# Performance work log

Hardware: AMD Instinct MI355X
Metric: run time of the kernel (lower is better)

Reference implementation:

```python
import jax, jax.numpy as jnp
import numpy as np

NUM_HEADS = 8
EPS = 1e-6


def setup_inputs() -> dict:
    key0 = jax.random.key(0)
    ks = jax.random.split(key0, 12)
    B, E, Hs, Ws, L = 8, 512, 32, 32, 1024
    s = 0.02
    return {
        "query": jax.random.normal(ks[0], (B, E, Hs, Ws), dtype=jnp.float32),
        "key": jax.random.normal(ks[1], (B, L, E), dtype=jnp.float32),
        "value": jax.random.normal(ks[2], (B, L, E), dtype=jnp.float32),
        # 1x1 conv for Q (kernel_size=1) stored as (E_out, E_in)
        "Wq": jax.random.normal(ks[3], (E, E), dtype=jnp.float32) * s,
        "bq": jnp.zeros((E,), dtype=jnp.float32),
        "Wk": jax.random.normal(ks[4], (E, E), dtype=jnp.float32) * s,
        "bk": jnp.zeros((E,), dtype=jnp.float32),
        "Wv": jax.random.normal(ks[5], (E, E), dtype=jnp.float32) * s,
        "bv": jnp.zeros((E,), dtype=jnp.float32),
        # out_conv: 1x1 conv + RMSNorm gain
        "Wo": jax.random.normal(ks[6], (E, E), dtype=jnp.float32) * s,
        "bo": jnp.zeros((E,), dtype=jnp.float32),
        "g": jnp.ones((E,), dtype=jnp.float32),
    }


def reference(query, key, value, Wq, bq, Wk, bk, Wv, bv, Wo, bo, g):
    B, E, Hs, Ws = query.shape
    H = NUM_HEADS
    Dh = E // H
    N = Hs * Ws
    # Q: 1x1 conv == per-pixel linear over channels
    Q = jnp.einsum('oi,bihw->bohw', Wq, query) + bq[None, :, None, None]
    # K, V: linear on last dim
    K = key @ Wk.T + bk      # (B, L, E)
    V = value @ Wv.T + bv    # (B, L, E)
    # faithful to torch .view: row-major reshape then transpose(2,3)
    Qh = Q.reshape(B, H, Dh, N).transpose(0, 1, 3, 2)        # (B, H, N, Dh)
    Kh = K.reshape(B, H, Dh, -1).transpose(0, 1, 3, 2)       # (B, H, L, Dh)
    Vh = V.reshape(B, H, Dh, -1).transpose(0, 1, 3, 2)       # (B, H, L, Dh)
    scores = jnp.einsum('bhnd,bhmd->bhnm', Qh, Kh) / jnp.sqrt(jnp.float32(Dh))
    attn = jax.nn.softmax(scores, axis=-1)
    out = jnp.einsum('bhnm,bhmd->bhnd', attn, Vh)            # (B, H, N, Dh)
    out = out.transpose(0, 1, 3, 2).reshape(B, E, Hs, Ws)
    # out_conv: 1x1 conv then channel-wise RMSNorm
    out = jnp.einsum('oi,bihw->bohw', Wo, out) + bo[None, :, None, None]
    rms = jnp.sqrt(jnp.mean(out * out, axis=1, keepdims=True) + EPS)
    return out / rms * g[None, :, None, None]
```

## Files before the change

### kernel.cpp

```cpp
#include <hip/hip_runtime.h>
#include <hip/hip_bf16.h>

namespace {

constexpr int kB  = 8;
constexpr int kE  = 512;
constexpr int kH  = 8;
constexpr int kDh = 64;
constexpr int kN  = 1024;
constexpr int kL  = 1024;

typedef __attribute__((ext_vector_type(8))) short short8;
typedef __attribute__((ext_vector_type(4))) float f32x4;
typedef __attribute__((ext_vector_type(4))) unsigned short ushort4v;

__device__ __forceinline__ unsigned short f2bf(float f) {
  unsigned u = __builtin_bit_cast(unsigned, f);
  u = (u + 0x7fffu + ((u >> 16) & 1u)) >> 16;
  return (unsigned short)u;
}

__device__ __forceinline__ f32x4 mfma16(short8 a, short8 b, f32x4 c) {
  return __builtin_amdgcn_mfma_f32_16x16x32_bf16(a, b, c, 0, 0, 0);
}

__device__ __forceinline__ void gl_lds16(const unsigned short* g, unsigned short* l) {
  __builtin_amdgcn_global_load_lds(
      (const __attribute__((address_space(1))) unsigned int*)g,
      (__attribute__((address_space(3))) unsigned int*)l, 16, 0, 0);
}

__global__ __launch_bounds__(256)
void convert_w(const float* __restrict__ w0, const float* __restrict__ w1,
               const float* __restrict__ w2, const float* __restrict__ w3,
               unsigned short* __restrict__ dst)
{
  const float* s = (blockIdx.y == 0) ? w0 : (blockIdx.y == 1) ? w1
                  : (blockIdx.y == 2) ? w2 : w3;
  unsigned short* d = dst + (size_t)blockIdx.y * 262144;
  const size_t i = ((size_t)blockIdx.x * 256 + threadIdx.x) * 4;
  const float4 v = *(const float4*)(s + i);
  ushort4v o = { f2bf(v.x), f2bf(v.y), f2bf(v.z), f2bf(v.w) };
  *(ushort4v*)(d + i) = o;
}

__global__ __launch_bounds__(256)
void convert_kv(const float* __restrict__ k, const float* __restrict__ v,
                unsigned short* __restrict__ dst)
{
  const float* s = blockIdx.y ? v : k;
  unsigned short* d = dst + (size_t)blockIdx.y * 4194304;
  const int flat = blockIdx.x * 256 + threadIdx.x;
  #pragma unroll
  for (int it = 0; it < 4; ++it) {
    const size_t i = ((size_t)flat + (size_t)it * 262144) * 4;
    const float4 x = *(const float4*)(s + i);
    ushort4v o = { f2bf(x.x), f2bf(x.y), f2bf(x.z), f2bf(x.w) };
    *(ushort4v*)(d + i) = o;
  }
}

__global__ __launch_bounds__(256)
void convert_qT(const float* __restrict__ q, unsigned short* __restrict__ qT)
{
  const int b = blockIdx.z, e0 = blockIdx.y * 32, n0 = blockIdx.x * 32;
  __shared__ float T[32][33];
  const int r  = threadIdx.x >> 3;
  const int c4 = (threadIdx.x & 7) * 4;
  const float4 v = *(const float4*)&q[((size_t)b * kE + e0 + r) * kN + n0 + c4];
  T[r][c4+0] = v.x; T[r][c4+1] = v.y; T[r][c4+2] = v.z; T[r][c4+3] = v.w;
  __syncthreads();
  ushort4v o = { f2bf(T[c4+0][r]), f2bf(T[c4+1][r]),
                 f2bf(T[c4+2][r]), f2bf(T[c4+3][r]) };
  *(ushort4v*)&qT[((size_t)b * kN + n0 + r) * kE + e0 + c4] = o;
}

__global__ __launch_bounds__(256)
void qkv_proj(const unsigned short* __restrict__ Wb4,
              const float* __restrict__ bq, const float* __restrict__ bk,
              const float* __restrict__ bv,
              const unsigned short* __restrict__ qT,
              const unsigned short* __restrict__ keyB,
              const unsigned short* __restrict__ valB,
              unsigned short* __restrict__ Qh,
              unsigned short* __restrict__ Kh,
              unsigned short* __restrict__ Vt)
{
  const int b    = blockIdx.z;
  const int mode = blockIdx.y >> 2;
  const int o0   = (blockIdx.y & 3) * 128;
  const int c0   = blockIdx.x * 128;
  const int wid  = threadIdx.x >> 6;
  const int lane = threadIdx.x & 63;
  const int lr = lane & 15, lg = lane >> 4;
  const int ow = o0 + (wid >> 1) * 64;
  const int cw = c0 + (wid & 1) * 64;

  __shared__ unsigned short Ts[18432];

  const unsigned short* Wb   = Wb4 + (size_t)mode * 262144;
  const float*          bias = (mode == 0) ? bq : (mode == 1) ? bk : bv;
  const unsigned short* X    = (mode == 0) ? qT : (mode == 1) ? keyB : valB;

  const unsigned short* Wp = Wb + (size_t)(ow + lr) * kE;
  const unsigned short* Xp = X + ((size_t)b * 1024 + cw + lr) * kE;

  const f32x4 z = {0.f, 0.f, 0.f, 0.f};
  f32x4 acc[4][4];
  #pragma unroll
  for (int i = 0; i < 4; ++i)
    #pragma unroll
    for (int j = 0; j < 4; ++j) acc[i][j] = z;

  for (int k0 = 0; k0 < kE; k0 += 32) {
    short8 a[4], bfr[4];
    #pragma unroll
    for (int fr = 0; fr < 4; ++fr)
      a[fr] = *(const short8*)(Wp + (size_t)fr * 16 * kE + k0 + lg * 8);
    #pragma unroll
    for (int fc = 0; fc < 4; ++fc)
      bfr[fc] = *(const short8*)(Xp + (size_t)fc * 16 * kE + k0 + lg * 8);
    #pragma unroll
    for (int fr = 0; fr < 4; ++fr)
      #pragma unroll
      for (int fc = 0; fc < 4; ++fc)
        acc[fr][fc] = mfma16(a[fr], bfr[fc], acc[fr][fc]);
  }

  #pragma unroll
  for (int fr = 0; fr < 4; ++fr) {
    #pragma unroll
    for (int j = 0; j < 4; ++j) {
      const int o  = ow + fr * 16 + 4 * lg + j;
      const int ol = o - o0;
      const float bvv = bias[o];
      #pragma unroll
      for (int fc = 0; fc < 4; ++fc) {
        const int cl = (cw - c0) + fc * 16 + lr;
        float val = acc[fr][fc][j] + bvv;
        int addr;
        if (mode == 0) {
          const int hl = ol >> 6, d = o & 63;
          const int r = hl * 128 + cl;
          addr = r * 72 + ((((d >> 3) ^ (r & 7)) << 3) | (d & 7));
          val *= 0.125f;
        } else if (mode == 1) {
          const int seg = cl & 1, d = cl >> 1;
          const int r = seg * 128 + ol;
          addr = r * 72 + ((((d >> 3) ^ (r & 7)) << 3) | (d & 7));
        } else {
          const int r = cl;
          addr = r * 136 + ((((ol >> 3) ^ (r & 15)) << 3) | (ol & 7));
        }
        Ts[addr] = f2bf(val);
      }
    }
  }
  __syncthreads();

  const int hseg = c0 >> 7;
  #pragma unroll
  for (int it = 0; it < 8; ++it) {
    const int q = it * 256 + threadIdx.x;
    if (mode != 2) {
      const int r = q >> 3, ch = q & 7;
      const short8 vv = *(const short8*)&Ts[r * 72 + ((ch ^ (r & 7)) << 3)];
      if (mode == 0) {
        const int hl = r >> 7, n = r & 127;
        *(short8*)&Qh[((size_t)(b * kH + (o0 >> 6) + hl) * kN + c0 + n) * kDh + ch * 8] = vv;
      } else {
        const int seg = r >> 7, ml = r & 127;
        *(short8*)&Kh[((size_t)(b * kH + hseg) * kL + seg * 512 + o0 + ml) * kDh + ch * 8] = vv;
      }
    } else {
      const int r = q >> 4, ch = q & 15;
      const short8 vv = *(const short8*)&Ts[r * 136 + ((ch ^ (r & 15)) << 3)];
      const int d = r >> 1, half = r & 1;
      *(short8*)&Vt[((size_t)(b * kH + hseg) * kDh + d) * kL + half * 512 + o0 + ch * 8] = vv;
    }
  }
}

__global__ __launch_bounds__(256)
void attn_mfma(const unsigned short* __restrict__ Qh,
               const unsigned short* __restrict__ Kh,
               const unsigned short* __restrict__ Vt,
               unsigned short* __restrict__ AO)
{
  const int bh = blockIdx.x;
  const int h = bh & 7, b = bh >> 3;
  const int n0 = blockIdx.y * 128;
  const int tid  = threadIdx.x;
  const int wid  = tid >> 6;
  const int lane = tid & 63;
  const int lr = lane & 15, lg = lane >> 4;

  __shared__ unsigned short Ks[2][64 * 64];
  __shared__ unsigned short Vs[2][64 * 64];
  __shared__ unsigned short Pst[4][2][16 * 72];

  const unsigned short* Qp = Qh + ((size_t)(b * kH + h) * kN + n0 + wid * 32) * kDh;
  const unsigned short* Kp = Kh + (size_t)(b * kH + h) * kL * kDh;
  const unsigned short* Vp = Vt + (size_t)(b * kH + h) * kDh * kL;

  short8 aq[2][2];
  #pragma unroll
  for (int rf = 0; rf < 2; ++rf) {
    aq[rf][0] = *(const short8*)(Qp + (size_t)(rf * 16 + lr) * kDh + lg * 8);
    aq[rf][1] = *(const short8*)(Qp + (size_t)(rf * 16 + lr) * kDh + 32 + lg * 8);
  }

  const int srow8 = lane >> 3;
  const int sc16  = lane & 7;

  auto stageK = [&](int buf, int m0) {
    #pragma unroll
    for (int c = 0; c < 2; ++c) {
      const int row = wid * 16 + c * 8 + srow8;
      const unsigned short* src =
          Kp + (size_t)(m0 + row) * kDh + ((sc16 ^ (row & 7)) << 3);
      gl_lds16(src, &Ks[buf][(wid * 16 + c * 8) * 64]);
    }
  };
  auto stageV = [&](int buf, int m0) {
    #pragma unroll
    for (int c = 0; c < 2; ++c) {
      const int row = wid * 16 + c * 8 + srow8;
      const unsigned short* src =
          Vp + (size_t)row * kL + m0 + ((sc16 ^ (row & 7)) << 3);
      gl_lds16(src, &Vs[buf][(wid * 16 + c * 8) * 64]);
    }
  };

  const f32x4 z = {0.f, 0.f, 0.f, 0.f};
  f32x4 oacc[2][4];
  #pragma unroll
  for (int rf = 0; rf < 2; ++rf)
    #pragma unroll
    for (int dt = 0; dt < 4; ++dt) oacc[rf][dt] = z;
  f32x4 psum[2] = {z, z};

  stageK(0, 0);
  stageV(0, 0);
  __syncthreads();

  for (int kt = 0; kt < 16; ++kt) {
    const int cur = kt & 1;
    if (kt < 15) {
      stageK(cur ^ 1, (kt + 1) * 64);
      stageV(cur ^ 1, (kt + 1) * 64);
    }

    #pragma unroll
    for (int rf = 0; rf < 2; ++rf) {
      f32x4 s[4] = {z, z, z, z};
      #pragma unroll
      for (int t = 0; t < 4; ++t) {
        const int row = t * 16 + lr;
        const short8 bk0 = *(const short8*)&Ks[cur][row * 64 + (((lg    ) ^ (row & 7)) << 3)];
        const short8 bk1 = *(const short8*)&Ks[cur][row * 64 + (((4 + lg) ^ (row & 7)) << 3)];
        s[t] = mfma16(aq[rf][0], bk0, s[t]);
        s[t] = mfma16(aq[rf][1], bk1, s[t]);
      }
      #pragma unroll
      for (int t = 0; t < 4; ++t)
        #pragma unroll
        for (int j = 0; j < 4; ++j) {
          const float p = __expf(s[t][j]);
          psum[rf][j] += p;
          Pst[wid][rf][(4 * lg + j) * 72 + 16 * t + lr] = f2bf(p);
        }
    }

    #pragma unroll
    for (int rf = 0; rf < 2; ++rf) {
      const short8 ap0 = *(const short8*)&Pst[wid][rf][lr * 72 + lg * 8];
      const short8 ap1 = *(const short8*)&Pst[wid][rf][lr * 72 + 32 + lg * 8];
      #pragma unroll
      for (int dt = 0; dt < 4; ++dt) {
        const int row = dt * 16 + lr;
        const short8 bv0 = *(const short8*)&Vs[cur][row * 64 + (((lg    ) ^ (row & 7)) << 3)];
        const short8 bv1 = *(const short8*)&Vs[cur][row * 64 + (((4 + lg) ^ (row & 7)) << 3)];
        oacc[rf][dt] = mfma16(ap0, bv0, oacc[rf][dt]);
        oacc[rf][dt] = mfma16(ap1, bv1, oacc[rf][dt]);
      }
    }

    __syncthreads();
  }

  #pragma unroll
  for (int rf = 0; rf < 2; ++rf)
    #pragma unroll
    for (int j = 0; j < 4; ++j) {
      float ps = psum[rf][j];
      ps += __shfl_xor(ps, 1);
      ps += __shfl_xor(ps, 2);
      ps += __shfl_xor(ps, 4);
      ps += __shfl_xor(ps, 8);
      psum[rf][j] = 1.0f / ps;
    }
  #pragma unroll
  for (int rf = 0; rf < 2; ++rf)
    #pragma unroll
    for (int dt = 0; dt < 4; ++dt)
      #pragma unroll
      for (int j = 0; j < 4; ++j) {
        const int n = n0 + wid * 32 + rf * 16 + 4 * lg + j;
        AO[((size_t)(b * kN + n)) * kE + h * kDh + dt * 16 + lr] =
            f2bf(oacc[rf][dt][j] * psum[rf][j]);
      }
}

__global__ __launch_bounds__(512)
void oproj_rms(const unsigned short* __restrict__ Wob, const float* __restrict__ bo,
               const unsigned short* __restrict__ AO, const float* __restrict__ g,
               float* __restrict__ out)
{
  const int b  = blockIdx.y;
  const int c0 = blockIdx.x * 32;
  const int wid  = threadIdx.x >> 6;
  const int lane = threadIdx.x & 63;
  const int lr = lane & 15, lg = lane >> 4;

  const unsigned short* Wp = Wob + (size_t)(wid * 64 + lr) * kE;
  const unsigned short* Xp = AO + ((size_t)b * kN + c0 + lr) * kE;

  const f32x4 z = {0.f, 0.f, 0.f, 0.f};
  f32x4 acc[4][2];
  #pragma unroll
  for (int i = 0; i < 4; ++i) { acc[i][0] = z; acc[i][1] = z; }

  for (int k0 = 0; k0 < kE; k0 += 32) {
    short8 a[4], bfr[2];
    #pragma unroll
    for (int fr = 0; fr < 4; ++fr)
      a[fr] = *(const short8*)(Wp + (size_t)fr * 16 * kE + k0 + lg * 8);
    #pragma unroll
    for (int fc = 0; fc < 2; ++fc)
      bfr[fc] = *(const short8*)(Xp + (size_t)fc * 16 * kE + k0 + lg * 8);
    #pragma unroll
    for (int fr = 0; fr < 4; ++fr)
      #pragma unroll
      for (int fc = 0; fc < 2; ++fc)
        acc[fr][fc] = mfma16(a[fr], bfr[fc], acc[fr][fc]);
  }

  float ss[2] = {0.f, 0.f};
  #pragma unroll
  for (int fr = 0; fr < 4; ++fr) {
    #pragma unroll
    for (int j = 0; j < 4; ++j) {
      const int o = wid * 64 + fr * 16 + 4 * lg + j;
      const float bvv = bo[o];
      #pragma unroll
      for (int fc = 0; fc < 2; ++fc) {
        const float v = acc[fr][fc][j] + bvv;
        acc[fr][fc][j] = v;
        ss[fc] = fmaf(v, v, ss[fc]);
      }
    }
  }
  #pragma unroll
  for (int fc = 0; fc < 2; ++fc) {
    ss[fc] += __shfl_xor(ss[fc], 16);
    ss[fc] += __shfl_xor(ss[fc], 32);
  }

  __shared__ float ssb[8][32];
  if (lg == 0) {
    ssb[wid][0 * 16 + lr] = ss[0];
    ssb[wid][1 * 16 + lr] = ss[1];
  }
  __syncthreads();

  float rinv[2];
  #pragma unroll
  for (int fc = 0; fc < 2; ++fc) {
    float tot = 0.f;
    #pragma unroll
    for (int w = 0; w < 8; ++w) tot += ssb[w][fc * 16 + lr];
    rinv[fc] = 1.0f / sqrtf(tot * (1.0f / 512.0f) + 1e-6f);
  }

  #pragma unroll
  for (int fr = 0; fr < 4; ++fr)
    #pragma unroll
    for (int j = 0; j < 4; ++j) {
      const int o = wid * 64 + fr * 16 + 4 * lg + j;
      const float gv = g[o];
      #pragma unroll
      for (int fc = 0; fc < 2; ++fc) {
        const int c = c0 + fc * 16 + lr;
        out[((size_t)b * kE + o) * kN + c] = acc[fr][fc][j] * rinv[fc] * gv;
      }
    }
}

}

extern "C" void kernel_launch(void* const* d_in, const int* in_sizes, int n_in,
                              void* d_out, int out_size, void* d_ws, size_t ws_size,
                              hipStream_t stream)
{
  const float* query = (const float*)d_in[0];
  const float* key   = (const float*)d_in[1];
  const float* value = (const float*)d_in[2];
  const float* Wq    = (const float*)d_in[3];
  const float* bq    = (const float*)d_in[4];
  const float* Wk    = (const float*)d_in[5];
  const float* bk    = (const float*)d_in[6];
  const float* Wv    = (const float*)d_in[7];
  const float* bv    = (const float*)d_in[8];
  const float* Wo    = (const float*)d_in[9];
  const float* bo    = (const float*)d_in[10];
  const float* g     = (const float*)d_in[11];
  float* out = (float*)d_out;

  char* w = (char*)d_ws;
  unsigned short* qT   = (unsigned short*)(w);
  unsigned short* keyB = (unsigned short*)(w + ((size_t)8 << 20));
  unsigned short* valB = (unsigned short*)(w + ((size_t)16 << 20));
  unsigned short* Qh   = (unsigned short*)(w + ((size_t)24 << 20));
  unsigned short* Kh   = (unsigned short*)(w + ((size_t)32 << 20));
  unsigned short* Vt   = (unsigned short*)(w + ((size_t)40 << 20));
  unsigned short* Wb   = (unsigned short*)(w + ((size_t)48 << 20));
  unsigned short* AO   = qT;

  const dim3 blk(256);
  convert_w <<<dim3(256, 4),    blk, 0, stream>>>(Wq, Wk, Wv, Wo, Wb);
  convert_kv<<<dim3(1024, 2),   blk, 0, stream>>>(key, value, keyB);
  convert_qT<<<dim3(32, 16, 8), blk, 0, stream>>>(query, qT);

  qkv_proj  <<<dim3(8, 12, 8),  blk, 0, stream>>>(Wb, bq, bk, bv, qT, keyB, valB,
                                                  Qh, Kh, Vt);
  attn_mfma <<<dim3(64, 8),     blk, 0, stream>>>(Qh, Kh, Vt, AO);
  oproj_rms <<<dim3(32, 8),     dim3(512), 0, stream>>>(Wb + 786432, bo, AO, g, out);
}
```

Measured before the change: 227.4 us.

## Stage QKV projection operands through double-buffered LDS with direct global-to-LDS loads

```diff
diff --git a/kernel.cpp b/kernel.cpp
--- a/kernel.cpp
+++ b/kernel.cpp
@@ -93,17 +93,32 @@
   const int wid  = threadIdx.x >> 6;
   const int lane = threadIdx.x & 63;
   const int lr = lane & 15, lg = lane >> 4;
-  const int ow = o0 + (wid >> 1) * 64;
-  const int cw = c0 + (wid & 1) * 64;
-
-  __shared__ unsigned short Ts[18432];
+  const int rbase = (wid >> 1) * 64;
+  const int cbase = (wid & 1) * 64;
+
+  __shared__ unsigned short smem[18432];
 
   const unsigned short* Wb   = Wb4 + (size_t)mode * 262144;
   const float*          bias = (mode == 0) ? bq : (mode == 1) ? bk : bv;
   const unsigned short* X    = (mode == 0) ? qT : (mode == 1) ? keyB : valB;
 
-  const unsigned short* Wp = Wb + (size_t)(ow + lr) * kE;
-  const unsigned short* Xp = X + ((size_t)b * 1024 + cw + lr) * kE;
+  const unsigned short* Wg = Wb + (size_t)o0 * kE;
+  const unsigned short* Xg = X + ((size_t)b * 1024 + c0) * kE;
+
+  const int srow = lane >> 2;
+  const int sch  = lane & 3;
+
+  auto stage = [&](int buf, int k0) {
+    #pragma unroll
+    for (int c = 0; c < 2; ++c) {
+      const int row = wid * 32 + c * 16 + srow;
+      const int koff = k0 + (((sch) ^ (row & 3)) << 3);
+      gl_lds16(Wg + (size_t)row * kE + koff,
+               &smem[buf * 8192 + (wid * 32 + c * 16) * 32]);
+      gl_lds16(Xg + (size_t)row * kE + koff,
+               &smem[buf * 8192 + 4096 + (wid * 32 + c * 16) * 32]);
+    }
+  };
 
   const f32x4 z = {0.f, 0.f, 0.f, 0.f};
   f32x4 acc[4][4];
@@ -112,31 +127,44 @@
     #pragma unroll
     for (int j = 0; j < 4; ++j) acc[i][j] = z;
 
-  for (int k0 = 0; k0 < kE; k0 += 32) {
+  stage(0, 0);
+  __syncthreads();
+
+  for (int kt = 0; kt < 16; ++kt) {
+    const int buf = kt & 1;
+    if (kt < 15) stage(buf ^ 1, (kt + 1) * 32);
+
     short8 a[4], bfr[4];
     #pragma unroll
-    for (int fr = 0; fr < 4; ++fr)
-      a[fr] = *(const short8*)(Wp + (size_t)fr * 16 * kE + k0 + lg * 8);
-    #pragma unroll
-    for (int fc = 0; fc < 4; ++fc)
-      bfr[fc] = *(const short8*)(Xp + (size_t)fc * 16 * kE + k0 + lg * 8);
+    for (int fr = 0; fr < 4; ++fr) {
+      const int row = rbase + fr * 16 + lr;
+      a[fr] = *(const short8*)&smem[buf * 8192 + row * 32 + ((lg ^ (row & 3)) << 3)];
+    }
+    #pragma unroll
+    for (int fc = 0; fc < 4; ++fc) {
+      const int row = cbase + fc * 16 + lr;
+      bfr[fc] = *(const short8*)&smem[buf * 8192 + 4096 + row * 32 + ((lg ^ (row & 3)) << 3)];
+    }
     #pragma unroll
     for (int fr = 0; fr < 4; ++fr)
       #pragma unroll
       for (int fc = 0; fc < 4; ++fc)
         acc[fr][fc] = mfma16(a[fr], bfr[fc], acc[fr][fc]);
-  }
-
+
+    __syncthreads();
+  }
+
+  unsigned short* Ts = smem;
   #pragma unroll
   for (int fr = 0; fr < 4; ++fr) {
     #pragma unroll
     for (int j = 0; j < 4; ++j) {
-      const int o  = ow + fr * 16 + 4 * lg + j;
-      const int ol = o - o0;
+      const int ol = rbase + fr * 16 + 4 * lg + j;
+      const int o  = o0 + ol;
       const float bvv = bias[o];
       #pragma unroll
       for (int fc = 0; fc < 4; ++fc) {
-        const int cl = (cw - c0) + fc * 16 + lr;
+        const int cl = cbase + fc * 16 + lr;
         float val = acc[fr][fc][j] + bvv;
         int addr;
         if (mode == 0) {
```

New measurement: 199.7 us. 12.2% less time.
